# Optimization experiments

Measured on AMD Instinct MI355X. Metric: run time of the kernel, lower is better.

## Reference

```python
import jax, jax.numpy as jnp
import numpy as np

MAT_MODE = ((0, 1), (0, 2), (1, 2))
VEC_MODE = (2, 1, 0)
DENSITY_SHIFT = -10.0
DISTANCE_SCALE = 25.0


def grid_sample_2d(img, coords):
    # img: [C, H, W]; coords: [N, 2] in [-1, 1], (x indexes W, y indexes H);
    # bilinear, align_corners=True (matches F.grid_sample in the source).
    C, H, W = img.shape
    x = (coords[:, 0] + 1.0) * 0.5 * (W - 1)
    y = (coords[:, 1] + 1.0) * 0.5 * (H - 1)
    x0 = jnp.floor(x)
    y0 = jnp.floor(y)
    wx = x - x0
    wy = y - y0
    x0i = jnp.clip(x0.astype(jnp.int32), 0, W - 1)
    x1i = jnp.clip(x0i + 1, 0, W - 1)
    y0i = jnp.clip(y0.astype(jnp.int32), 0, H - 1)
    y1i = jnp.clip(y0i + 1, 0, H - 1)
    v00 = img[:, y0i, x0i]
    v01 = img[:, y0i, x1i]
    v10 = img[:, y1i, x0i]
    v11 = img[:, y1i, x1i]
    return (v00 * (1 - wx) * (1 - wy) + v01 * wx * (1 - wy)
            + v10 * (1 - wx) * wy + v11 * wx * wy)  # [C, N]


def line_sample_1d(line, t):
    # line: [C, L]; t: [N] in [-1, 1]. Equivalent to the source's grid_sample on a
    # [1, C, L, 1] tensor with coords (0, t): the width dim (size 1) collapses.
    C, L = line.shape
    y = (t + 1.0) * 0.5 * (L - 1)
    y0 = jnp.floor(y)
    wy = y - y0
    y0i = jnp.clip(y0.astype(jnp.int32), 0, L - 1)
    y1i = jnp.clip(y0i + 1, 0, L - 1)
    return line[:, y0i] * (1 - wy) + line[:, y1i] * wy  # [C, N]


def tensorf_features(planes, lines, xyz):
    # planes: [3, C, H, W]; lines: [3, C, L]; xyz: [N, 3] normalized coords.
    # fusion_two='concat' then fusion_one='multiply' == per-plane multiply, concat.
    feats = []
    for i in range(3):
        a, b = MAT_MODE[i]
        pc = jnp.stack([xyz[:, a], xyz[:, b]], axis=-1)  # [N, 2]
        pf = grid_sample_2d(planes[i], pc)               # [C, N]
        lf = line_sample_1d(lines[i], xyz[:, VEC_MODE[i]])  # [C, N]
        feats.append(pf * lf)
    return jnp.concatenate(feats, axis=0)  # [3C, N]


def raw2alpha(sigma, dist):
    # sigma, dist: [Nr, Ns]
    alpha = 1.0 - jnp.exp(-sigma * dist)
    T = jnp.cumprod(jnp.concatenate(
        [jnp.ones((alpha.shape[0], 1), alpha.dtype), 1.0 - alpha + 1e-10], axis=-1), axis=-1)
    weights = alpha * T[:, :-1]
    return alpha, weights, T[:, -1:]


def setup_inputs() -> dict:
    key = jax.random.key(0)
    ks = jax.random.split(key, 10)
    Nr, Ns, G = 4096, 256, 300
    aabb = jnp.array([[-1.5, -1.5, -1.5], [1.5, 1.5, 1.5]], jnp.float32)
    xyz_sampled = jax.random.uniform(ks[0], (Nr, Ns, 3), jnp.float32,
                                     minval=-1.5, maxval=1.5)
    vd = jax.random.normal(ks[1], (Nr, 3), jnp.float32)
    viewdirs = vd / jnp.linalg.norm(vd, axis=-1, keepdims=True)
    near, far = 2.0, 6.0
    t = jnp.linspace(0.0, 1.0, Ns, dtype=jnp.float32)
    z_vals = near * (1.0 - t) + far * t
    z_vals = jnp.broadcast_to(z_vals, (Nr, Ns)) + \
        jax.random.uniform(ks[2], (Nr, Ns), jnp.float32) * ((far - near) / Ns)
    z_vals = jnp.sort(z_vals, axis=-1)
    s = 0.1  # init_scale
    return {
        'xyz_sampled': xyz_sampled,
        'viewdirs': viewdirs,
        'z_vals': z_vals,
        'density_planes': s * jax.random.normal(ks[3], (3, 8, G, G), jnp.float32),
        'density_lines': s * jax.random.normal(ks[4], (3, 8, G), jnp.float32),
        'app_planes': s * jax.random.normal(ks[5], (3, 24, G, G), jnp.float32),
        'app_lines': s * jax.random.normal(ks[6], (3, 24, G), jnp.float32),
        'density_basis_w': jnp.ones((1, 24), jnp.float32),  # source inits to 1/density_dim
        'app_basis_w': s * jax.random.normal(ks[7], (3, 72), jnp.float32),
        'aabb': aabb,
    }


def reference(xyz_sampled, viewdirs, z_vals, density_planes, density_lines,
              app_planes, app_lines, density_basis_w, app_basis_w, aabb):
    Nr, Ns, _ = xyz_sampled.shape
    # normalize_coord: map aabb -> [-1, 1]
    inv_size = 2.0 / (aabb[1] - aabb[0])
    xyz = ((xyz_sampled - aabb[0]) * inv_size - 1.0).reshape(-1, 3)  # [N, 3]

    dfeat = tensorf_features(density_planes, density_lines, xyz)      # [24, N]
    sigma_feat = (density_basis_w @ dfeat).reshape(Nr, Ns)            # basis_mat
    sigma = jax.nn.softplus(sigma_feat + DENSITY_SHIFT)               # fea2denseAct

    # ray-marching distances
    dists = z_vals[:, 1:] - z_vals[:, :-1]
    dists = jnp.concatenate([dists, dists[:, -1:]], axis=-1)
    alpha, weights, bg_T = raw2alpha(sigma, dists * DISTANCE_SCALE)

    # appearance branch: RGBRender is identity on the 3-dim basis output
    afeat = tensorf_features(app_planes, app_lines, xyz)              # [72, N]
    rgb = (app_basis_w @ afeat).T.reshape(Nr, Ns, 3)

    rgb_map = jnp.sum(weights[..., None] * rgb, axis=1)               # [Nr, 3]
    return rgb_map
```

## Files before the change

kernel.cpp:

```cpp
#include <hip/hip_runtime.h>
#include <math.h>

#define G  300
#define NS 256
#define NR 4096
#define CT 32
#define SLABS 4

typedef _Float16 half16_t;
typedef _Float16 h8 __attribute__((ext_vector_type(8)));

__global__ __launch_bounds__(256) void prep_all(
    const float* __restrict__ dp, const float* __restrict__ ap,
    const float* __restrict__ dl, const float* __restrict__ al,
    half16_t* __restrict__ outp, half16_t* __restrict__ outl)
{
  int t = blockIdx.x * blockDim.x + threadIdx.x;
  if (t < 3 * G * G) {
    int x  = t % G;
    int yi = t / G;
    int y  = yi % G;
    int i  = yi / G;
    const float* dpp = dp + ((size_t)(i * 8) * G + y) * G + x;
    const float* app = ap + ((size_t)(i * 24) * G + y) * G + x;
    h8 v[4];
#pragma unroll
    for (int c = 0; c < 8; ++c) v[c >> 3][c & 7] = (half16_t)dpp[(size_t)c * G * G];
#pragma unroll
    for (int c = 0; c < 24; ++c) {
      int cc = c + 8;
      v[cc >> 3][cc & 7] = (half16_t)app[(size_t)c * G * G];
    }
    h8* o = (h8*)(outp + (size_t)t * CT);
#pragma unroll
    for (int m = 0; m < 4; ++m) o[m] = v[m];
  } else {
    int u = t - 3 * G * G;
    if (u < 3 * G) {
      int p = u % G;
      int i = u / G;
      h8 v[4];
#pragma unroll
      for (int c = 0; c < 8; ++c) v[c >> 3][c & 7] = (half16_t)dl[(i * 8 + c) * G + p];
#pragma unroll
      for (int c = 0; c < 24; ++c) {
        int cc = c + 8;
        v[cc >> 3][cc & 7] = (half16_t)al[(i * 24 + c) * G + p];
      }
      h8* o = (h8*)(outl + (size_t)u * CT);
#pragma unroll
      for (int m = 0; m < 4; ++m) o[m] = v[m];
    }
  }
}

__global__ __launch_bounds__(256) void tensorf_fused(
    const float* __restrict__ xyz, const float* __restrict__ zv,
    const half16_t* __restrict__ planes, const half16_t* __restrict__ lns,
    const float* __restrict__ dbw, const float* __restrict__ abw,
    const float* __restrict__ aabb, float* __restrict__ out)
{
  __shared__ float4 srgb[4][NS];
  __shared__ unsigned char lst[4][2][SLABS][NS];
  __shared__ float sW[3][128];

  const int tid = threadIdx.x;
  for (int idx = tid; idx < 3 * 128; idx += 256) {
    int j = idx >> 7, c = idx & 127;
    float v = 0.f;
    if (c < 72) v = abw[j * 72 + c];
    else if (j == 0 && c < 96) v = dbw[c - 72];
    sW[j][c] = v;
  }

  const int wv   = tid >> 6;
  const int lane = tid & 63;
  const int ray  = (blockIdx.x << 2) + wv;
  const int q    = lane >> 2;
  const int r    = lane & 3;

#pragma unroll
  for (int j = 0; j < 4; ++j) srgb[wv][(lane << 2) + j] = make_float4(0.f, 0.f, 0.f, 0.f);

  const float a0x = aabb[0], a0y = aabb[1], a0z = aabb[2];
  const float ivx = 2.f / (aabb[3] - aabb[0]);
  const float ivy = 2.f / (aabb[4] - aabb[1]);
  const float ivz = 2.f / (aabb[5] - aabb[2]);
  const float A0[3] = {a0x, a0y, a0z};
  const float IV[3] = {ivx, ivy, ivz};

  __syncthreads();

  int o0[SLABS] = {0, 0, 0, 0};
  int o1[SLABS] = {0, 0, 0, 0};
  {
    const float slabScale = (float)SLABS / (float)G;
    int key0[4], key1[4];
#pragma unroll
    for (int j = 0; j < 4; ++j) {
      int s = (lane << 2) + j;
      const float* xp = xyz + ((size_t)ray * NS + s) * 3;
      float g1 = (xp[1] - a0y) * ivy - 1.f;
      float g2 = (xp[2] - a0z) * ivz - 1.f;
      float fy0 = (g1 + 1.f) * (0.5f * (G - 1));
      float fy1 = (g2 + 1.f) * (0.5f * (G - 1));
      key0[j] = min(max((int)(fy0 * slabScale), 0), SLABS - 1);
      key1[j] = min(max((int)(fy1 * slabScale), 0), SLABS - 1);
    }
    const unsigned long long ltmask = (1ull << lane) - 1ull;
#pragma unroll
    for (int j = 0; j < 4; ++j) {
      int s = (lane << 2) + j;
#pragma unroll
      for (int k = 0; k < SLABS; ++k) {
        unsigned long long m0 = __ballot(key0[j] == k);
        if (key0[j] == k)
          lst[wv][0][k][o0[k] + __popcll(m0 & ltmask)] = (unsigned char)s;
        o0[k] += (int)__popcll(m0);
        unsigned long long m1 = __ballot(key1[j] == k);
        if (key1[j] == k)
          lst[wv][1][k][o1[k] + __popcll(m1 & ltmask)] = (unsigned char)s;
        o1[k] += (int)__popcll(m1);
      }
    }
  }
  __syncthreads();

  const int MA[3] = {0, 0, 1};
  const int MB[3] = {1, 2, 2};
  const int MV[3] = {2, 1, 0};
  const int ro = r * 8;

#pragma unroll
  for (int p = 0; p < 3; ++p) {
    const int li = (p == 0) ? 0 : 1;
    const half16_t* pb = planes + (size_t)p * G * G * CT;
    const half16_t* lb = lns + (size_t)p * G * CT + ro;
    const int cb = (r == 0) ? (72 + p * 8) : (p * 24 + (r - 1) * 8);
    const float4 W0a = *(const float4*)&sW[0][cb];
    const float4 W0b = *(const float4*)&sW[0][cb + 4];
    const float4 W1a = *(const float4*)&sW[1][cb];
    const float4 W1b = *(const float4*)&sW[1][cb + 4];
    const float4 W2a = *(const float4*)&sW[2][cb];
    const float4 W2b = *(const float4*)&sW[2][cb + 4];

#pragma unroll
    for (int sl = 0; sl < SLABS; ++sl) {
      const int n = min((li == 0) ? o0[sl] : o1[sl], NS);
      for (int base = 0; base < n; base += 16) {
        int e = base + q;
        if (e < n) {
          int sid = lst[wv][li][sl][e];
          const float* xp = xyz + ((size_t)ray * NS + sid) * 3;
          float ga = (xp[MA[p]] - A0[MA[p]]) * IV[MA[p]] - 1.f;
          float gb = (xp[MB[p]] - A0[MB[p]]) * IV[MB[p]] - 1.f;
          float gv = (xp[MV[p]] - A0[MV[p]]) * IV[MV[p]] - 1.f;
          float fx = (ga + 1.f) * (0.5f * (G - 1));
          float fy = (gb + 1.f) * (0.5f * (G - 1));
          float ft = (gv + 1.f) * (0.5f * (G - 1));

          float x0f = floorf(fx), y0f = floorf(fy), t0f = floorf(ft);
          float wx = fx - x0f, wy = fy - y0f, wt = ft - t0f;
          int x0 = min(max((int)x0f, 0), G - 1);
          int y0 = min(max((int)y0f, 0), G - 1);
          int t0 = min(max((int)t0f, 0), G - 1);
          int x1 = min(x0 + 1, G - 1);
          int y1 = min(y0 + 1, G - 1);
          int t1 = min(t0 + 1, G - 1);

          h8 t00 = *(const h8*)(pb + ((size_t)(y0 * G + x0)) * CT + ro);
          h8 t01 = *(const h8*)(pb + ((size_t)(y0 * G + x1)) * CT + ro);
          h8 t10 = *(const h8*)(pb + ((size_t)(y1 * G + x0)) * CT + ro);
          h8 t11 = *(const h8*)(pb + ((size_t)(y1 * G + x1)) * CT + ro);
          h8 l0  = *(const h8*)(lb + (size_t)t0 * CT);
          h8 l1  = *(const h8*)(lb + (size_t)t1 * CT);

          float w00 = (1.f - wx) * (1.f - wy), w01 = wx * (1.f - wy);
          float w10 = (1.f - wx) * wy,         w11 = wx * wy;
          float wl0 = 1.f - wt;

          float f[8];
#pragma unroll
          for (int k = 0; k < 8; ++k) {
            float pf = (float)t00[k] * w00 + (float)t01[k] * w01
                     + (float)t10[k] * w10 + (float)t11[k] * w11;
            float lf = (float)l0[k] * wl0 + (float)l1[k] * wt;
            f[k] = pf * lf;
          }
          float acc0 = W0a.x * f[0] + W0a.y * f[1] + W0a.z * f[2] + W0a.w * f[3]
                     + W0b.x * f[4] + W0b.y * f[5] + W0b.z * f[6] + W0b.w * f[7];
          float acc1 = W1a.x * f[0] + W1a.y * f[1] + W1a.z * f[2] + W1a.w * f[3]
                     + W1b.x * f[4] + W1b.y * f[5] + W1b.z * f[6] + W1b.w * f[7];
          float acc2 = W2a.x * f[0] + W2a.y * f[1] + W2a.z * f[2] + W2a.w * f[3]
                     + W2b.x * f[4] + W2b.y * f[5] + W2b.z * f[6] + W2b.w * f[7];

          float4 v;
          v.x = (r == 0) ? acc0 : 0.f;
          v.y = (r == 0) ? 0.f : acc0;
          v.z = (r == 0) ? 0.f : acc1;
          v.w = (r == 0) ? 0.f : acc2;
#pragma unroll
          for (int m = 1; m <= 2; m <<= 1) {
            v.x += __shfl_xor(v.x, m);
            v.y += __shfl_xor(v.y, m);
            v.z += __shfl_xor(v.z, m);
            v.w += __shfl_xor(v.w, m);
          }
          if (r == 0) {
            float4 a = srgb[wv][sid];
            a.x += v.x; a.y += v.y; a.z += v.z; a.w += v.w;
            srgb[wv][sid] = a;
          }
        }
      }
    }
  }

  const float* zp = zv + (size_t)ray * NS + (lane << 2);
  float4 z4 = *(const float4*)zp;
  float znext = __shfl_down(z4.x, 1);
  float d[4];
  d[0] = z4.y - z4.x;
  d[1] = z4.z - z4.y;
  d[2] = z4.w - z4.z;
  d[3] = (lane == 63) ? d[2] : (znext - z4.w);

  float4 c[4];
  float al[4];
  float tl = 1.f;
#pragma unroll
  for (int j = 0; j < 4; ++j) {
    c[j] = srgb[wv][(lane << 2) + j];
    float vs = c[j].x - 10.0f;
    float sp = (vs > 0.f) ? (vs + log1pf(expf(-vs))) : log1pf(expf(vs));
    al[j] = 1.f - expf(-sp * (d[j] * 25.0f));
    tl *= (1.f - al[j] + 1e-10f);
  }
  float incl = tl;
#pragma unroll
  for (int off = 1; off < 64; off <<= 1) {
    float pp = __shfl_up(incl, off);
    if (lane >= off) incl *= pp;
  }
  float T = __shfl_up(incl, 1);
  if (lane == 0) T = 1.f;

  float ar = 0.f, ag = 0.f, ab = 0.f;
#pragma unroll
  for (int j = 0; j < 4; ++j) {
    float w = al[j] * T;
    ar += w * c[j].y;
    ag += w * c[j].z;
    ab += w * c[j].w;
    T *= (1.f - al[j] + 1e-10f);
  }
#pragma unroll
  for (int off = 32; off > 0; off >>= 1) {
    ar += __shfl_down(ar, off);
    ag += __shfl_down(ag, off);
    ab += __shfl_down(ab, off);
  }
  if (lane == 0) {
    out[ray * 3 + 0] = ar;
    out[ray * 3 + 1] = ag;
    out[ray * 3 + 2] = ab;
  }
}

extern "C" void kernel_launch(void* const* d_in, const int* in_sizes, int n_in,
                              void* d_out, int out_size, void* d_ws, size_t ws_size,
                              hipStream_t stream)
{
  const float* xyz  = (const float*)d_in[0];
  const float* zv   = (const float*)d_in[2];
  const float* dp   = (const float*)d_in[3];
  const float* dl   = (const float*)d_in[4];
  const float* ap   = (const float*)d_in[5];
  const float* al   = (const float*)d_in[6];
  const float* dbw  = (const float*)d_in[7];
  const float* abw  = (const float*)d_in[8];
  const float* aabb = (const float*)d_in[9];
  float* outp = (float*)d_out;

  half16_t* planes16 = (half16_t*)d_ws;
  half16_t* lines16  = planes16 + (size_t)3 * G * G * CT;

  hipLaunchKernelGGL(prep_all, dim3((3 * G * G + 3 * G + 255) / 256), dim3(256), 0, stream,
                     dp, ap, dl, al, planes16, lines16);
  hipLaunchKernelGGL(tensorf_fused, dim3(NR / 4), dim3(256), 0, stream,
                     xyz, zv, planes16, lines16, dbw, abw, aabb, outp);
}
```

Before: 220.2 us.

## Sort samples once by 2D slab key and fuse all three planes per sample

Replaces the per-plane 1D slab binning (two separate sample lists) with a single list sorted by a combined 6x6 slab key over the y and z coordinates. Each sample is then processed once for all three planes, accumulating density and rgb in registers and writing the result straight to shared memory without read-modify-write. Normalized coordinates are cached in shared memory so they are not reloaded from global memory. This aims to cut loop overhead, partially empty 16-sample iterations, repeated xyz loads and shared accumulation traffic, at the cost of weaker locality for plane 0 and a longer 36-bucket ballot sort.

```diff
diff --git a/kernel.cpp b/kernel.cpp
--- a/kernel.cpp
+++ b/kernel.cpp
@@ -5,7 +5,7 @@
 #define NS 256
 #define NR 4096
 #define CT 32
-#define SLABS 4
+#define SLABS 6
 
 typedef _Float16 half16_t;
 typedef _Float16 h8 __attribute__((ext_vector_type(8)));
@@ -61,7 +61,8 @@
     const float* __restrict__ aabb, float* __restrict__ out)
 {
   __shared__ float4 srgb[4][NS];
-  __shared__ unsigned char lst[4][2][SLABS][NS];
+  __shared__ float4 sG[4][NS];
+  __shared__ unsigned char lst[4][NS];
   __shared__ float sW[3][128];
 
   const int tid = threadIdx.x;
@@ -79,48 +80,41 @@
   const int q    = lane >> 2;
   const int r    = lane & 3;
 
-#pragma unroll
-  for (int j = 0; j < 4; ++j) srgb[wv][(lane << 2) + j] = make_float4(0.f, 0.f, 0.f, 0.f);
-
   const float a0x = aabb[0], a0y = aabb[1], a0z = aabb[2];
   const float ivx = 2.f / (aabb[3] - aabb[0]);
   const float ivy = 2.f / (aabb[4] - aabb[1]);
   const float ivz = 2.f / (aabb[5] - aabb[2]);
-  const float A0[3] = {a0x, a0y, a0z};
-  const float IV[3] = {ivx, ivy, ivz};
-
-  __syncthreads();
-
-  int o0[SLABS] = {0, 0, 0, 0};
-  int o1[SLABS] = {0, 0, 0, 0};
+
+  int key[4];
   {
     const float slabScale = (float)SLABS / (float)G;
-    int key0[4], key1[4];
 #pragma unroll
     for (int j = 0; j < 4; ++j) {
       int s = (lane << 2) + j;
       const float* xp = xyz + ((size_t)ray * NS + s) * 3;
+      float g0 = (xp[0] - a0x) * ivx - 1.f;
       float g1 = (xp[1] - a0y) * ivy - 1.f;
       float g2 = (xp[2] - a0z) * ivz - 1.f;
+      sG[wv][s] = make_float4(g0, g1, g2, 0.f);
       float fy0 = (g1 + 1.f) * (0.5f * (G - 1));
       float fy1 = (g2 + 1.f) * (0.5f * (G - 1));
-      key0[j] = min(max((int)(fy0 * slabScale), 0), SLABS - 1);
-      key1[j] = min(max((int)(fy1 * slabScale), 0), SLABS - 1);
-    }
+      int k0 = min(max((int)(fy0 * slabScale), 0), SLABS - 1);
+      int k1 = min(max((int)(fy1 * slabScale), 0), SLABS - 1);
+      key[j] = k0 * SLABS + k1;
+    }
+  }
+
+  {
     const unsigned long long ltmask = (1ull << lane) - 1ull;
-#pragma unroll
-    for (int j = 0; j < 4; ++j) {
-      int s = (lane << 2) + j;
-#pragma unroll
-      for (int k = 0; k < SLABS; ++k) {
-        unsigned long long m0 = __ballot(key0[j] == k);
-        if (key0[j] == k)
-          lst[wv][0][k][o0[k] + __popcll(m0 & ltmask)] = (unsigned char)s;
-        o0[k] += (int)__popcll(m0);
-        unsigned long long m1 = __ballot(key1[j] == k);
-        if (key1[j] == k)
-          lst[wv][1][k][o1[k] + __popcll(m1 & ltmask)] = (unsigned char)s;
-        o1[k] += (int)__popcll(m1);
+    int off = 0;
+    for (int b = 0; b < SLABS * SLABS; ++b) {
+#pragma unroll
+      for (int j = 0; j < 4; ++j) {
+        bool hit = (key[j] == b);
+        unsigned long long m = __ballot(hit);
+        if (hit) lst[wv][off + (int)__popcll(m & ltmask)] =
+                   (unsigned char)((lane << 2) + j);
+        off += (int)__popcll(m);
       }
     }
   }
@@ -131,90 +125,79 @@
   const int MV[3] = {2, 1, 0};
   const int ro = r * 8;
 
-#pragma unroll
-  for (int p = 0; p < 3; ++p) {
-    const int li = (p == 0) ? 0 : 1;
-    const half16_t* pb = planes + (size_t)p * G * G * CT;
-    const half16_t* lb = lns + (size_t)p * G * CT + ro;
-    const int cb = (r == 0) ? (72 + p * 8) : (p * 24 + (r - 1) * 8);
-    const float4 W0a = *(const float4*)&sW[0][cb];
-    const float4 W0b = *(const float4*)&sW[0][cb + 4];
-    const float4 W1a = *(const float4*)&sW[1][cb];
-    const float4 W1b = *(const float4*)&sW[1][cb + 4];
-    const float4 W2a = *(const float4*)&sW[2][cb];
-    const float4 W2b = *(const float4*)&sW[2][cb + 4];
-
-#pragma unroll
-    for (int sl = 0; sl < SLABS; ++sl) {
-      const int n = min((li == 0) ? o0[sl] : o1[sl], NS);
-      for (int base = 0; base < n; base += 16) {
-        int e = base + q;
-        if (e < n) {
-          int sid = lst[wv][li][sl][e];
-          const float* xp = xyz + ((size_t)ray * NS + sid) * 3;
-          float ga = (xp[MA[p]] - A0[MA[p]]) * IV[MA[p]] - 1.f;
-          float gb = (xp[MB[p]] - A0[MB[p]]) * IV[MB[p]] - 1.f;
-          float gv = (xp[MV[p]] - A0[MV[p]]) * IV[MV[p]] - 1.f;
-          float fx = (ga + 1.f) * (0.5f * (G - 1));
-          float fy = (gb + 1.f) * (0.5f * (G - 1));
-          float ft = (gv + 1.f) * (0.5f * (G - 1));
-
-          float x0f = floorf(fx), y0f = floorf(fy), t0f = floorf(ft);
-          float wx = fx - x0f, wy = fy - y0f, wt = ft - t0f;
-          int x0 = min(max((int)x0f, 0), G - 1);
-          int y0 = min(max((int)y0f, 0), G - 1);
-          int t0 = min(max((int)t0f, 0), G - 1);
-          int x1 = min(x0 + 1, G - 1);
-          int y1 = min(y0 + 1, G - 1);
-          int t1 = min(t0 + 1, G - 1);
-
-          h8 t00 = *(const h8*)(pb + ((size_t)(y0 * G + x0)) * CT + ro);
-          h8 t01 = *(const h8*)(pb + ((size_t)(y0 * G + x1)) * CT + ro);
-          h8 t10 = *(const h8*)(pb + ((size_t)(y1 * G + x0)) * CT + ro);
-          h8 t11 = *(const h8*)(pb + ((size_t)(y1 * G + x1)) * CT + ro);
-          h8 l0  = *(const h8*)(lb + (size_t)t0 * CT);
-          h8 l1  = *(const h8*)(lb + (size_t)t1 * CT);
-
-          float w00 = (1.f - wx) * (1.f - wy), w01 = wx * (1.f - wy);
-          float w10 = (1.f - wx) * wy,         w11 = wx * wy;
-          float wl0 = 1.f - wt;
-
-          float f[8];
-#pragma unroll
-          for (int k = 0; k < 8; ++k) {
-            float pf = (float)t00[k] * w00 + (float)t01[k] * w01
-                     + (float)t10[k] * w10 + (float)t11[k] * w11;
-            float lf = (float)l0[k] * wl0 + (float)l1[k] * wt;
-            f[k] = pf * lf;
-          }
-          float acc0 = W0a.x * f[0] + W0a.y * f[1] + W0a.z * f[2] + W0a.w * f[3]
-                     + W0b.x * f[4] + W0b.y * f[5] + W0b.z * f[6] + W0b.w * f[7];
-          float acc1 = W1a.x * f[0] + W1a.y * f[1] + W1a.z * f[2] + W1a.w * f[3]
-                     + W1b.x * f[4] + W1b.y * f[5] + W1b.z * f[6] + W1b.w * f[7];
-          float acc2 = W2a.x * f[0] + W2a.y * f[1] + W2a.z * f[2] + W2a.w * f[3]
-                     + W2b.x * f[4] + W2b.y * f[5] + W2b.z * f[6] + W2b.w * f[7];
-
-          float4 v;
-          v.x = (r == 0) ? acc0 : 0.f;
-          v.y = (r == 0) ? 0.f : acc0;
-          v.z = (r == 0) ? 0.f : acc1;
-          v.w = (r == 0) ? 0.f : acc2;
-#pragma unroll
-          for (int m = 1; m <= 2; m <<= 1) {
-            v.x += __shfl_xor(v.x, m);
-            v.y += __shfl_xor(v.y, m);
-            v.z += __shfl_xor(v.z, m);
-            v.w += __shfl_xor(v.w, m);
-          }
-          if (r == 0) {
-            float4 a = srgb[wv][sid];
-            a.x += v.x; a.y += v.y; a.z += v.z; a.w += v.w;
-            srgb[wv][sid] = a;
-          }
-        }
+  for (int base = 0; base < NS; base += 16) {
+    int sid = lst[wv][base + q];
+    float4 g4 = sG[wv][sid];
+    float g[3] = {g4.x, g4.y, g4.z};
+
+    float acc0 = 0.f, acc1 = 0.f, acc2 = 0.f;
+#pragma unroll
+    for (int i = 0; i < 3; ++i) {
+      float fx = (g[MA[i]] + 1.f) * (0.5f * (G - 1));
+      float fy = (g[MB[i]] + 1.f) * (0.5f * (G - 1));
+      float ft = (g[MV[i]] + 1.f) * (0.5f * (G - 1));
+      float x0f = floorf(fx), y0f = floorf(fy), t0f = floorf(ft);
+      float wx = fx - x0f, wy = fy - y0f, wt = ft - t0f;
+      int x0 = min(max((int)x0f, 0), G - 1);
+      int y0 = min(max((int)y0f, 0), G - 1);
+      int t0 = min(max((int)t0f, 0), G - 1);
+      int x1 = min(x0 + 1, G - 1);
+      int y1 = min(y0 + 1, G - 1);
+      int t1 = min(t0 + 1, G - 1);
+
+      const half16_t* pb = planes + (size_t)i * G * G * CT;
+      h8 t00 = *(const h8*)(pb + ((size_t)(y0 * G + x0)) * CT + ro);
+      h8 t01 = *(const h8*)(pb + ((size_t)(y0 * G + x1)) * CT + ro);
+      h8 t10 = *(const h8*)(pb + ((size_t)(y1 * G + x0)) * CT + ro);
+      h8 t11 = *(const h8*)(pb + ((size_t)(y1 * G + x1)) * CT + ro);
+      const half16_t* lb = lns + (size_t)i * G * CT + ro;
+      h8 l0 = *(const h8*)(lb + (size_t)t0 * CT);
+      h8 l1 = *(const h8*)(lb + (size_t)t1 * CT);
+
+      float w00 = (1.f - wx) * (1.f - wy), w01 = wx * (1.f - wy);
+      float w10 = (1.f - wx) * wy,         w11 = wx * wy;
+      float wl0 = 1.f - wt;
+
+      float f[8];
+#pragma unroll
+      for (int k = 0; k < 8; ++k) {
+        float pf = (float)t00[k] * w00 + (float)t01[k] * w01
+                 + (float)t10[k] * w10 + (float)t11[k] * w11;
+        float lf = (float)l0[k] * wl0 + (float)l1[k] * wt;
+        f[k] = pf * lf;
       }
-    }
-  }
+
+      int cb = (r == 0) ? (72 + i * 8) : (i * 24 + (r - 1) * 8);
+      const float4* wp0 = (const float4*)&sW[0][cb];
+      const float4* wp1 = (const float4*)&sW[1][cb];
+      const float4* wp2 = (const float4*)&sW[2][cb];
+      float4 wa, wb;
+      wa = wp0[0]; wb = wp0[1];
+      acc0 += wa.x * f[0] + wa.y * f[1] + wa.z * f[2] + wa.w * f[3]
+            + wb.x * f[4] + wb.y * f[5] + wb.z * f[6] + wb.w * f[7];
+      wa = wp1[0]; wb = wp1[1];
+      acc1 += wa.x * f[0] + wa.y * f[1] + wa.z * f[2] + wa.w * f[3]
+            + wb.x * f[4] + wb.y * f[5] + wb.z * f[6] + wb.w * f[7];
+      wa = wp2[0]; wb = wp2[1];
+      acc2 += wa.x * f[0] + wa.y * f[1] + wa.z * f[2] + wa.w * f[3]
+            + wb.x * f[4] + wb.y * f[5] + wb.z * f[6] + wb.w * f[7];
+    }
+
+    float4 v;
+    v.x = (r == 0) ? acc0 : 0.f;
+    v.y = (r == 0) ? 0.f : acc0;
+    v.z = (r == 0) ? 0.f : acc1;
+    v.w = (r == 0) ? 0.f : acc2;
+#pragma unroll
+    for (int m = 1; m <= 2; m <<= 1) {
+      v.x += __shfl_xor(v.x, m);
+      v.y += __shfl_xor(v.y, m);
+      v.z += __shfl_xor(v.z, m);
+      v.w += __shfl_xor(v.w, m);
+    }
+    if (r == 0) srgb[wv][sid] = v;
+  }
+  __syncthreads();
 
   const float* zp = zv + (size_t)ray * NS + (lane << 2);
   float4 z4 = *(const float4*)zp;
```

Measured after the change: 214.6 us, median of 2. 1.03x faster.
